# Kernel optimization log

Hardware: AMD Instinct MI355X
Metric: run time of the kernel (lower is better)

## Reference

```python
import jax, jax.numpy as jnp
import numpy as np

NUM_CLASSES = 3
POS_T, NEG_T = 0.5, 0.3
RATIO = 3
W_OBJ, W_CLS, W_LOC = 1.0, 1.0, 2.0


def _pairwise_iou(a, b):
    # a: [N,4] anchors, b: [G,4] gt boxes, xyxy
    ix1 = jnp.maximum(a[:, None, 0], b[None, :, 0])
    iy1 = jnp.maximum(a[:, None, 1], b[None, :, 1])
    ix2 = jnp.minimum(a[:, None, 2], b[None, :, 2])
    iy2 = jnp.minimum(a[:, None, 3], b[None, :, 3])
    inter = jnp.clip(ix2 - ix1, 0) * jnp.clip(iy2 - iy1, 0)
    area_a = (a[:, 2] - a[:, 0]) * (a[:, 3] - a[:, 1])
    area_b = (b[:, 2] - b[:, 0]) * (b[:, 3] - b[:, 1])
    union = area_a[:, None] + area_b[None, :] - inter
    return inter / jnp.maximum(union, 1e-9)


def _masked_mean(x, m):
    c = m.sum()
    return jnp.where(c > 0, (x * m).sum() / jnp.maximum(c, 1.0), 0.0)


def _per_image(pred, anc, ax, ay, aw, ah, boxes_gt, labels_gt):
    # pred: [N, 5+nc]; anc: [N,4]; boxes_gt: [G,4]; labels_gt: [G] in 1..nc
    iou = _pairwise_iou(anc, boxes_gt)              # [N, G]
    best = jnp.argmax(iou, axis=1)
    best_iou = jnp.max(iou, axis=1)
    pos = best_iou >= POS_T
    neg = best_iou < NEG_T
    mb = boxes_gt[best]                             # matched boxes [N,4]
    ml = labels_gt[best]                            # matched labels [N]
    obj_logit = pred[:, 4]
    cls_logit = pred[:, 5:]
    obj_t = pos.astype(pred.dtype)
    # BCEWithLogits (numerically stable)
    obj_loss = jnp.maximum(obj_logit, 0) - obj_logit * obj_t + jnp.log1p(jnp.exp(-jnp.abs(obj_logit)))
    # hard negative mining: top-(3*num_pos) detached obj losses among negatives
    num_pos = pos.sum()
    k = jnp.minimum(RATIO * num_pos, neg.sum())
    cand = jnp.where(neg, jax.lax.stop_gradient(obj_loss), -1.0)
    order = jnp.argsort(-cand)
    ranks = jnp.zeros_like(order).at[order].set(jnp.arange(order.shape[0], dtype=order.dtype))
    sel_neg = neg & (ranks < k)
    loss_obj = _masked_mean(obj_loss, (pos | sel_neg).astype(pred.dtype))
    # classification over positives, labels shifted to 0-based
    logp = jax.nn.log_softmax(cls_logit, axis=-1)
    tgt = jnp.clip(ml - 1, 0)
    ce = -jnp.take_along_axis(logp, tgt[:, None], axis=1)[:, 0]
    loss_cls = _masked_mean(ce, pos.astype(pred.dtype))
    # localization over positives: SmoothL1 on encoded offsets
    gx = (mb[:, 0] + mb[:, 2]) * 0.5
    gy = (mb[:, 1] + mb[:, 3]) * 0.5
    gw = jnp.maximum(mb[:, 2] - mb[:, 0], 1e-6)
    gh = jnp.maximum(mb[:, 3] - mb[:, 1], 1e-6)
    loc_tgt = jnp.stack([(gx - ax) / aw, (gy - ay) / ah,
                         jnp.log(gw / aw), jnp.log(gh / ah)], axis=1)
    d = pred[:, :4] - loc_tgt
    ad = jnp.abs(d)
    sl1 = jnp.where(ad < 1.0, 0.5 * d * d, ad - 0.5)  # [N,4]
    pm = pos.astype(pred.dtype)
    cnt = 4.0 * pm.sum()
    loss_loc = jnp.where(cnt > 0, (sl1 * pm[:, None]).sum() / jnp.maximum(cnt, 1.0), 0.0)
    return loss_obj, loss_cls, loss_loc


def _detection_loss(preds, ancs, gt_boxes, gt_labels):
    B = preds[0].shape[0]
    obj_s = 0.0
    cls_s = 0.0
    loc_s = 0.0
    for pred, anc in zip(preds, ancs):
        Bp, C, H, W = pred.shape
        p = jnp.transpose(pred, (0, 2, 3, 1)).reshape(Bp, -1, 5 + NUM_CLASSES)
        ax = (anc[:, 0] + anc[:, 2]) * 0.5
        ay = (anc[:, 1] + anc[:, 3]) * 0.5
        aw = jnp.maximum(anc[:, 2] - anc[:, 0], 1e-6)
        ah = jnp.maximum(anc[:, 3] - anc[:, 1], 1e-6)
        lo, lc, ll = jax.vmap(
            lambda pb, bb, lb: _per_image(pb, anc, ax, ay, aw, ah, bb, lb)
        )(p, gt_boxes, gt_labels)
        obj_s = obj_s + lo.sum()
        cls_s = cls_s + lc.sum()
        loc_s = loc_s + ll.sum()
    obj_m = obj_s / B
    cls_m = cls_s / B
    loc_m = loc_s / B
    total = W_OBJ * obj_m + W_CLS * cls_m + W_LOC * loc_m
    return total, obj_m, cls_m, loc_m


def setup_inputs() -> dict:
    key = jax.random.key(0)
    k = jax.random.split(key, 8)
    B, G, A = 32, 50, 3
    img = 512.0
    scales = [(128, 128), (64, 64), (32, 32)]
    C = A * (5 + NUM_CLASSES)  # 24

    def make_anchors(H, W):
        stride = img / H
        ys, xs = np.meshgrid(np.arange(H), np.arange(W), indexing="ij")
        cx = (xs + 0.5) * stride
        cy = (ys + 0.5) * stride
        per = []
        for s in (1.0, 1.5, 2.0):
            half = s * stride
            per.append(np.stack([cx - half, cy - half, cx + half, cy + half], axis=-1).reshape(-1, 4))
        b = np.stack(per, axis=1).reshape(-1, 4)  # [H*W*A, 4], A innermost
        return jnp.asarray(b, dtype=jnp.float32)

    preds = [jax.random.normal(k[i], (B, C, H, W), dtype=jnp.float32) for i, (H, W) in enumerate(scales)]
    ancs = [make_anchors(H, W) for (H, W) in scales]
    cx = jax.random.uniform(k[3], (B, G)) * 384.0 + 64.0
    cy = jax.random.uniform(k[4], (B, G)) * 384.0 + 64.0
    w = jax.random.uniform(k[5], (B, G)) * 112.0 + 16.0
    h = jax.random.uniform(k[6], (B, G)) * 112.0 + 16.0
    gt_boxes = jnp.stack([cx - w / 2, cy - h / 2, cx + w / 2, cy + h / 2], axis=-1).astype(jnp.float32)
    gt_labels = jax.random.randint(k[7], (B, G), 1, NUM_CLASSES + 1)
    return {"p0": preds[0], "p1": preds[1], "p2": preds[2],
            "a0": ancs[0], "a1": ancs[1], "a2": ancs[2],
            "gt_boxes": gt_boxes, "gt_labels": gt_labels}


def reference(p0, p1, p2, a0, a1, a2, gt_boxes, gt_labels):
    return _detection_loss([p0, p1, p2], [a0, a1, a2], gt_boxes, gt_labels)
```

## Files before the change

### kernel.cpp

```cpp
#include <hip/hip_runtime.h>

#define WS_ACC_POS   0
#define WS_ACC_NEG   96
#define WS_ACC_OBJ   192
#define WS_ACC_CLS   288
#define WS_ACC_LOC   384
#define WS_SENT      480
#define WS_H1        512
#define WS_TOTAL_U32 (512 + 96*192*2)

#define NBINS        192
#define BIN_OFF      872
#define SUM_SCALE    33554432.0f
#define INV_SUM_SCALE (1.0f/33554432.0f)

__device__ __forceinline__ float sl1f(float d){
  float ad = fabsf(d); return ad < 1.f ? 0.5f*d*d : ad - 0.5f;
}
__device__ __forceinline__ unsigned int rec_cnt(unsigned int v){
  return (v >= 0xA0000000u) ? (v - 0xAAAAAAAAu) : v;
}

__global__ __launch_bounds__(256) void k_main(
    const float* __restrict__ p0, const float* __restrict__ p1, const float* __restrict__ p2,
    const float* __restrict__ gtb, const int* __restrict__ gtl,
    unsigned int* __restrict__ ws)
{
  const int id = blockIdx.x;
  int s, bIm, chunk, H, lw; const float* p;
  if (id < 2048){ s=0; H=128; lw=7; chunk=id>>5;            bIm=id&31;          p=p0; }
  else if (id < 2560){ s=1; H=64; lw=6; chunk=(id-2048)>>5; bIm=(id-2048)&31;   p=p1; }
  else {              s=2; H=32; lw=5; chunk=(id-2560)>>5;  bIm=(id-2560)&31;   p=p2; }
  const int W = H, HW = H*W;
  const float stride = 512.0f/(float)H;
  const int g = s*32 + bIm;
  const int tid = threadIdx.x;

  __shared__ float4 sBox[52];
  __shared__ float  sArea[52], sGx[52], sGy[52], sGw[52], sGh[52];
  __shared__ int    sLbl[52];
  __shared__ int    sNk;
  __shared__ unsigned long long sH[NBINS];
  __shared__ float  sRF[3][4];
  __shared__ unsigned int sRU[2][4];

  if (tid < 64){
    const int ymin = (chunk*256)>>lw;
    const int rowc = 256>>lw;
    const float by1 = ((float)ymin+0.5f)*stride - 2.0f*stride;
    const float by2 = ((float)(ymin+rowc-1)+0.5f)*stride + 2.0f*stride;
    bool keep=false; float4 gb=make_float4(0,0,0,0); int lbl=0;
    if (tid < 50){
      gb  = *(const float4*)(gtb + ((size_t)bIm*50 + tid)*4);
      lbl = gtl[bIm*50 + tid];
      keep = (fminf(by2, gb.w) - fmaxf(by1, gb.y)) > 0.f;
    }
    unsigned long long m = __ballot(keep);
    if (keep){
      int idx = __popcll(m & ((1ull<<tid)-1ull));
      sBox[idx]=gb;
      sArea[idx]=(gb.z-gb.x)*(gb.w-gb.y);
      sGx[idx]=(gb.x+gb.z)*0.5f;  sGy[idx]=(gb.y+gb.w)*0.5f;
      sGw[idx]=fmaxf(gb.z-gb.x,1e-6f); sGh[idx]=fmaxf(gb.w-gb.y,1e-6f);
      sLbl[idx]=lbl;
    }
    if (tid==0) sNk = __popcll(m);
  }
  if (tid < NBINS) sH[tid]=0ull;
  __syncthreads();

  const int nk = sNk;
  const int hw  = chunk*256 + tid;
  const int hwW = chunk*256 + (tid & ~63);
  const int y = hw>>lw, x = hw&(W-1);
  const float cx = ((float)x+0.5f)*stride, cy = ((float)y+0.5f)*stride;

  const float* pb = p + (size_t)bIm*24*HW + hw;
  float xo[3];
  #pragma unroll
  for (int a=0;a<3;a++) xo[a] = pb[(size_t)(a*8+4)*HW];

  const int wxlo = (W >= 64) ? (hwW & (W-1)) : 0;
  const int wxhi = (W >= 64) ? (wxlo + 63)   : (W-1);
  const int wylo = hwW>>lw, wyhi = (hwW+63)>>lw;
  const float m2 = 2.0f*stride;
  const float wx1 = ((float)wxlo+0.5f)*stride - m2;
  const float wx2 = ((float)wxhi+0.5f)*stride + m2;
  const float wy1 = ((float)wylo+0.5f)*stride - m2;
  const float wy2 = ((float)wyhi+0.5f)*stride + m2;

  float half[3]; half[0]=stride; half[1]=1.5f*stride; half[2]=2.0f*stride;
  float areaA[3], bi[3], bu[3]; int bj[3];
  #pragma unroll
  for (int a=0;a<3;a++){
    const float aw = 2.0f*half[a];
    areaA[a]=aw*aw; bi[a]=0.f; bu[a]=1e-9f; bj[a]=0;
  }
  for (int j=0;j<nk;j++){
    const float4 gb = sBox[j];
    if (gb.x >= wx2 || gb.z <= wx1 || gb.y >= wy2 || gb.w <= wy1) continue;
    const float ar = sArea[j];
    #pragma unroll
    for (int a=0;a<3;a++){
      const float iy1 = fmaxf(cy-half[a], gb.y), iy2 = fminf(cy+half[a], gb.w);
      const float ih  = fmaxf(iy2-iy1, 0.f);
      const float ix1 = fmaxf(cx-half[a], gb.x), ix2 = fminf(cx+half[a], gb.z);
      const float iw  = fmaxf(ix2-ix1, 0.f);
      const float inter = iw*ih;
      const float un = areaA[a] + ar - inter;
      if (inter*bu[a] > bi[a]*un){ bi[a]=inter; bu[a]=un; bj[a]=j; }
    }
  }

  int accPos=0, accNeg=0;
  float accObj=0.f, accCls=0.f, accLoc=0.f;
  #pragma unroll
  for (int a=0;a<3;a++){
    const float bestIou = bi[a]/bu[a];
    const bool pos = bestIou >= 0.5f;
    const bool neg = bestIou < 0.3f;
    if (pos || neg){
      float objl = fmaxf(xo[a],0.f) - (pos ? xo[a] : 0.f)
                 + __logf(1.f + __expf(-fabsf(xo[a])));
      objl = fmaxf(objl, 0.f);
      if (neg){
        accNeg++;
        const int bin = min(max((int)(__float_as_uint(objl)>>20) - BIN_OFF, 0), NBINS-1);
        const unsigned long long pack =
            (1ull<<48) | (unsigned long long)__float2uint_rn(objl * SUM_SCALE);
        atomicAdd(&sH[bin], pack);
      } else {
        accPos++; accObj += objl;
        const int jb = bj[a];
        const float aw = 2.0f*half[a];
        const float c0=pb[(size_t)(a*8+5)*HW], c1=pb[(size_t)(a*8+6)*HW], c2=pb[(size_t)(a*8+7)*HW];
        const float mm = fmaxf(fmaxf(c0,c1),c2);
        const float lse = mm + __logf(__expf(c0-mm)+__expf(c1-mm)+__expf(c2-mm));
        const int t = max(sLbl[jb]-1, 0);
        const float ct = (t==0)?c0 : (t==1)?c1 : c2;
        accCls += lse - ct;
        const float tx = (sGx[jb]-cx)/aw;
        const float ty = (sGy[jb]-cy)/aw;
        const float tw = __logf(sGw[jb]/aw);
        const float th = __logf(sGh[jb]/aw);
        accLoc += sl1f(pb[(size_t)(a*8+0)*HW]-tx) + sl1f(pb[(size_t)(a*8+1)*HW]-ty)
                + sl1f(pb[(size_t)(a*8+2)*HW]-tw) + sl1f(pb[(size_t)(a*8+3)*HW]-th);
      }
    }
  }

  #pragma unroll
  for (int o=32;o;o>>=1){
    accPos += __shfl_down(accPos,o,64);
    accNeg += __shfl_down(accNeg,o,64);
    accObj += __shfl_down(accObj,o,64);
    accCls += __shfl_down(accCls,o,64);
    accLoc += __shfl_down(accLoc,o,64);
  }
  if ((tid & 63)==0){
    const int w = tid>>6;
    sRU[0][w]=(unsigned)accPos; sRU[1][w]=(unsigned)accNeg;
    sRF[0][w]=accObj; sRF[1][w]=accCls; sRF[2][w]=accLoc;
  }
  __syncthreads();
  if (tid==0){
    float* wf = (float*)ws;
    unsigned pc=0, nc=0; float ob=0,cl=0,lc=0;
    #pragma unroll
    for (int w=0;w<4;w++){ pc+=sRU[0][w]; nc+=sRU[1][w]; ob+=sRF[0][w]; cl+=sRF[1][w]; lc+=sRF[2][w]; }
    if (pc) atomicAdd(&ws[WS_ACC_POS+g], pc);
    if (nc) atomicAdd(&ws[WS_ACC_NEG+g], nc);
    if (ob!=0.f) atomicAdd(&wf[WS_ACC_OBJ+g], ob);
    if (cl!=0.f) atomicAdd(&wf[WS_ACC_CLS+g], cl);
    if (lc!=0.f) atomicAdd(&wf[WS_ACC_LOC+g], lc);
  }
  if (tid < NBINS){
    const unsigned long long v = sH[tid];
    if (v){
      unsigned long long* gH = (unsigned long long*)(ws + WS_H1) + (size_t)g*NBINS;
      atomicAdd(&gH[tid], v);
    }
  }
}

__global__ __launch_bounds__(64) void k_select(unsigned int* __restrict__ ws,
                                               float* __restrict__ out){
  const int g = blockIdx.x, lane = threadIdx.x;
  float* wf = (float*)ws;
  __shared__ int   sTie, sR;
  __shared__ float sTieAvg;

  const int pos  = (int)rec_cnt(ws[WS_ACC_POS+g]);
  const int negc = (int)rec_cnt(ws[WS_ACC_NEG+g]);
  const int k = min(3*pos, negc);
  float selSum = 0.f;

  if (k > 0){
    const unsigned long long base =
        (ws[WS_SENT]==0xAAAAAAAAu) ? 0xAAAAAAAAAAAAAAAAull : 0ull;
    const unsigned long long* gH =
        (const unsigned long long*)(ws + WS_H1) + (size_t)g*NBINS;
    unsigned int c[3]; float sm[3];
    #pragma unroll
    for (int j=0;j<3;j++){
      const unsigned long long d = gH[lane*3+j] - base;
      c[j]  = (unsigned int)(d>>48);
      sm[j] = (float)(d & 0xFFFFFFFFFFFFull) * INV_SUM_SCALE;
    }
    const unsigned int c3 = c[0]+c[1]+c[2];
    unsigned int incl = c3;
    #pragma unroll
    for (int off=1; off<64; off<<=1){
      unsigned int yv = __shfl_down(incl, off, 64);
      if (lane+off < 64) incl += yv;
    }
    const unsigned int excl = incl - c3;
    if (lane==0){ sTie = -1; sR = 0; sTieAvg = 0.f; }
    if (excl < (unsigned)k && incl >= (unsigned)k){
      unsigned int cum = excl;
      #pragma unroll
      for (int j=2;j>=0;j--){
        const unsigned int cc = c[j];
        if (cum + cc >= (unsigned)k){
          sTie = lane*3+j; sR = (int)((unsigned)k - cum);
          sTieAvg = sm[j]/(float)cc;
          break;
        }
        cum += cc;
      }
    }
    __syncthreads();
    const int tie = sTie;
    float above = 0.f;
    #pragma unroll
    for (int j=0;j<3;j++) if (lane*3+j > tie) above += sm[j];
    #pragma unroll
    for (int o=32;o;o>>=1) above += __shfl_down(above,o,64);
    selSum = above + (float)sR * sTieAvg;
  }
  if (lane==0){
    const int cObj = pos + k;
    const float lo = (cObj>0) ? (wf[WS_ACC_OBJ+g]+selSum)/(float)cObj : 0.f;
    const float lc = (pos>0)  ? wf[WS_ACC_CLS+g]/(float)pos           : 0.f;
    const float ll = (pos>0)  ? wf[WS_ACC_LOC+g]/(float)(4*pos)       : 0.f;
    const float invB = 1.f/32.f;
    atomicAdd(out+0, (lo + lc + 2.f*ll)*invB);
    atomicAdd(out+1, lo*invB);
    atomicAdd(out+2, lc*invB);
    atomicAdd(out+3, ll*invB);
  }
}

extern "C" void kernel_launch(void* const* d_in, const int* in_sizes, int n_in,
                              void* d_out, int out_size, void* d_ws, size_t ws_size,
                              hipStream_t stream){
  if (ws_size < (size_t)WS_TOTAL_U32*4) return;
  const float* p0  = (const float*)d_in[0];
  const float* p1  = (const float*)d_in[1];
  const float* p2  = (const float*)d_in[2];
  const float* gtb = (const float*)d_in[6];
  const int*   gtl = (const int*)d_in[7];
  unsigned int* ws = (unsigned int*)d_ws;
  float* out = (float*)d_out;

  hipLaunchKernelGGL(k_main,   dim3(2688), dim3(256), 0, stream, p0,p1,p2,gtb,gtl,ws);
  hipLaunchKernelGGL(k_select, dim3(96),   dim3(64),  0, stream, ws, out);
}
```

Measured before the change: 122.6 us.

## Process two horizontal pixels per thread with float2 loads, halving grid size

Each thread now handles two adjacent x positions, loading the objectness logits as float2 and reusing the per-gt-box y-overlap and box fetch across both pixels. The grid is halved to match, and each block now covers twice as many rows. The wave-level gt culling drops its x-range test and keeps only the y-range test, so more boxes may go through the IoU loop. The change aims to cut shared-memory box loads, per-block setup and block count, at the cost of more registers per thread and less parallelism.

```diff
diff --git a/kernel.cpp b/kernel.cpp
--- a/kernel.cpp
+++ b/kernel.cpp
@@ -28,10 +28,11 @@
 {
   const int id = blockIdx.x;
   int s, bIm, chunk, H, lw; const float* p;
-  if (id < 2048){ s=0; H=128; lw=7; chunk=id>>5;            bIm=id&31;          p=p0; }
-  else if (id < 2560){ s=1; H=64; lw=6; chunk=(id-2048)>>5; bIm=(id-2048)&31;   p=p1; }
-  else {              s=2; H=32; lw=5; chunk=(id-2560)>>5;  bIm=(id-2560)&31;   p=p2; }
+  if (id < 1024){ s=0; H=128; lw=7; chunk=id>>5;            bIm=id&31;          p=p0; }
+  else if (id < 1280){ s=1; H=64; lw=6; chunk=(id-1024)>>5; bIm=(id-1024)&31;   p=p1; }
+  else {              s=2; H=32; lw=5; chunk=(id-1280)>>5;  bIm=(id-1280)&31;   p=p2; }
   const int W = H, HW = H*W;
+  const int lwp = lw-1, halfW = W>>1;
   const float stride = 512.0f/(float)H;
   const int g = s*32 + bIm;
   const int tid = threadIdx.x;
@@ -45,10 +46,10 @@
   __shared__ unsigned int sRU[2][4];
 
   if (tid < 64){
-    const int ymin = (chunk*256)>>lw;
-    const int rowc = 256>>lw;
+    const int R = 512>>lw;
+    const int ymin = chunk*R;
     const float by1 = ((float)ymin+0.5f)*stride - 2.0f*stride;
-    const float by2 = ((float)(ymin+rowc-1)+0.5f)*stride + 2.0f*stride;
+    const float by2 = ((float)(ymin+R-1)+0.5f)*stride + 2.0f*stride;
     bool keep=false; float4 gb=make_float4(0,0,0,0); int lbl=0;
     if (tid < 50){
       gb  = *(const float4*)(gtb + ((size_t)bIm*50 + tid)*4);
@@ -70,81 +71,92 @@
   __syncthreads();
 
   const int nk = sNk;
-  const int hw  = chunk*256 + tid;
-  const int hwW = chunk*256 + (tid & ~63);
-  const int y = hw>>lw, x = hw&(W-1);
-  const float cx = ((float)x+0.5f)*stride, cy = ((float)y+0.5f)*stride;
-
-  const float* pb = p + (size_t)bIm*24*HW + hw;
-  float xo[3];
-  #pragma unroll
-  for (int a=0;a<3;a++) xo[a] = pb[(size_t)(a*8+4)*HW];
-
-  const int wxlo = (W >= 64) ? (hwW & (W-1)) : 0;
-  const int wxhi = (W >= 64) ? (wxlo + 63)   : (W-1);
-  const int wylo = hwW>>lw, wyhi = (hwW+63)>>lw;
+  const int pairIdx = chunk*256 + tid;
+  const int y  = pairIdx>>lwp;
+  const int x0 = (pairIdx & (halfW-1))<<1;
+  const int hw0 = y*W + x0;
+  const float cx0 = ((float)x0+0.5f)*stride, cy = ((float)y+0.5f)*stride;
+
+  const float* pb = p + (size_t)bIm*24*HW + hw0;
+  float2 xo2[3];
+  #pragma unroll
+  for (int a=0;a<3;a++) xo2[a] = *(const float2*)(pb + (size_t)(a*8+4)*HW);
+
+  const int wbase = chunk*256 + (tid & ~63);
+  const int ylo = wbase>>lwp, yhi = (wbase+63)>>lwp;
   const float m2 = 2.0f*stride;
-  const float wx1 = ((float)wxlo+0.5f)*stride - m2;
-  const float wx2 = ((float)wxhi+0.5f)*stride + m2;
-  const float wy1 = ((float)wylo+0.5f)*stride - m2;
-  const float wy2 = ((float)wyhi+0.5f)*stride + m2;
+  const float wy1 = ((float)ylo+0.5f)*stride - m2;
+  const float wy2 = ((float)yhi+0.5f)*stride + m2;
 
   float half[3]; half[0]=stride; half[1]=1.5f*stride; half[2]=2.0f*stride;
-  float areaA[3], bi[3], bu[3]; int bj[3];
+  float areaA[3], bi[2][3], bu[2][3]; int bj[2][3];
   #pragma unroll
   for (int a=0;a<3;a++){
     const float aw = 2.0f*half[a];
-    areaA[a]=aw*aw; bi[a]=0.f; bu[a]=1e-9f; bj[a]=0;
+    areaA[a]=aw*aw;
+    #pragma unroll
+    for (int i=0;i<2;i++){ bi[i][a]=0.f; bu[i][a]=1e-9f; bj[i][a]=0; }
   }
   for (int j=0;j<nk;j++){
     const float4 gb = sBox[j];
-    if (gb.x >= wx2 || gb.z <= wx1 || gb.y >= wy2 || gb.w <= wy1) continue;
+    if (gb.y >= wy2 || gb.w <= wy1) continue;
     const float ar = sArea[j];
     #pragma unroll
     for (int a=0;a<3;a++){
       const float iy1 = fmaxf(cy-half[a], gb.y), iy2 = fminf(cy+half[a], gb.w);
       const float ih  = fmaxf(iy2-iy1, 0.f);
-      const float ix1 = fmaxf(cx-half[a], gb.x), ix2 = fminf(cx+half[a], gb.z);
-      const float iw  = fmaxf(ix2-ix1, 0.f);
-      const float inter = iw*ih;
-      const float un = areaA[a] + ar - inter;
-      if (inter*bu[a] > bi[a]*un){ bi[a]=inter; bu[a]=un; bj[a]=j; }
+      #pragma unroll
+      for (int i=0;i<2;i++){
+        const float cxi = cx0 + (float)i*stride;
+        const float ix1 = fmaxf(cxi-half[a], gb.x), ix2 = fminf(cxi+half[a], gb.z);
+        const float iw  = fmaxf(ix2-ix1, 0.f);
+        const float inter = iw*ih;
+        const float un = areaA[a] + ar - inter;
+        if (inter*bu[i][a] > bi[i][a]*un){ bi[i][a]=inter; bu[i][a]=un; bj[i][a]=j; }
+      }
     }
   }
 
   int accPos=0, accNeg=0;
   float accObj=0.f, accCls=0.f, accLoc=0.f;
   #pragma unroll
-  for (int a=0;a<3;a++){
-    const float bestIou = bi[a]/bu[a];
-    const bool pos = bestIou >= 0.5f;
-    const bool neg = bestIou < 0.3f;
-    if (pos || neg){
-      float objl = fmaxf(xo[a],0.f) - (pos ? xo[a] : 0.f)
-                 + __logf(1.f + __expf(-fabsf(xo[a])));
-      objl = fmaxf(objl, 0.f);
-      if (neg){
-        accNeg++;
-        const int bin = min(max((int)(__float_as_uint(objl)>>20) - BIN_OFF, 0), NBINS-1);
-        const unsigned long long pack =
-            (1ull<<48) | (unsigned long long)__float2uint_rn(objl * SUM_SCALE);
-        atomicAdd(&sH[bin], pack);
-      } else {
-        accPos++; accObj += objl;
-        const int jb = bj[a];
-        const float aw = 2.0f*half[a];
-        const float c0=pb[(size_t)(a*8+5)*HW], c1=pb[(size_t)(a*8+6)*HW], c2=pb[(size_t)(a*8+7)*HW];
-        const float mm = fmaxf(fmaxf(c0,c1),c2);
-        const float lse = mm + __logf(__expf(c0-mm)+__expf(c1-mm)+__expf(c2-mm));
-        const int t = max(sLbl[jb]-1, 0);
-        const float ct = (t==0)?c0 : (t==1)?c1 : c2;
-        accCls += lse - ct;
-        const float tx = (sGx[jb]-cx)/aw;
-        const float ty = (sGy[jb]-cy)/aw;
-        const float tw = __logf(sGw[jb]/aw);
-        const float th = __logf(sGh[jb]/aw);
-        accLoc += sl1f(pb[(size_t)(a*8+0)*HW]-tx) + sl1f(pb[(size_t)(a*8+1)*HW]-ty)
-                + sl1f(pb[(size_t)(a*8+2)*HW]-tw) + sl1f(pb[(size_t)(a*8+3)*HW]-th);
+  for (int i=0;i<2;i++){
+    const int hw = hw0 + i;
+    const float cxi = cx0 + (float)i*stride;
+    const float* pbi = pb + i;
+    #pragma unroll
+    for (int a=0;a<3;a++){
+      const float bestIou = bi[i][a]/bu[i][a];
+      const bool pos = bestIou >= 0.5f;
+      const bool neg = bestIou < 0.3f;
+      if (pos || neg){
+        const float xo = (i==0) ? xo2[a].x : xo2[a].y;
+        float objl = fmaxf(xo,0.f) - (pos ? xo : 0.f)
+                   + __logf(1.f + __expf(-fabsf(xo)));
+        objl = fmaxf(objl, 0.f);
+        if (neg){
+          accNeg++;
+          const int bin = min(max((int)(__float_as_uint(objl)>>20) - BIN_OFF, 0), NBINS-1);
+          const unsigned long long pack =
+              (1ull<<48) | (unsigned long long)__float2uint_rn(objl * SUM_SCALE);
+          atomicAdd(&sH[bin], pack);
+        } else {
+          accPos++; accObj += objl;
+          const int jb = bj[i][a];
+          const float aw = 2.0f*half[a];
+          const float c0=pbi[(size_t)(a*8+5)*HW], c1=pbi[(size_t)(a*8+6)*HW], c2=pbi[(size_t)(a*8+7)*HW];
+          const float mm = fmaxf(fmaxf(c0,c1),c2);
+          const float lse = mm + __logf(__expf(c0-mm)+__expf(c1-mm)+__expf(c2-mm));
+          const int t = max(sLbl[jb]-1, 0);
+          const float ct = (t==0)?c0 : (t==1)?c1 : c2;
+          accCls += lse - ct;
+          const float tx = (sGx[jb]-cxi)/aw;
+          const float ty = (sGy[jb]-cy )/aw;
+          const float tw = __logf(sGw[jb]/aw);
+          const float th = __logf(sGh[jb]/aw);
+          accLoc += sl1f(pbi[(size_t)(a*8+0)*HW]-tx) + sl1f(pbi[(size_t)(a*8+1)*HW]-ty)
+                  + sl1f(pbi[(size_t)(a*8+2)*HW]-tw) + sl1f(pbi[(size_t)(a*8+3)*HW]-th);
+        }
       }
     }
   }
@@ -263,6 +275,6 @@
   unsigned int* ws = (unsigned int*)d_ws;
   float* out = (float*)d_out;
 
-  hipLaunchKernelGGL(k_main,   dim3(2688), dim3(256), 0, stream, p0,p1,p2,gtb,gtl,ws);
+  hipLaunchKernelGGL(k_main,   dim3(1344), dim3(256), 0, stream, p0,p1,p2,gtb,gtl,ws);
   hipLaunchKernelGGL(k_select, dim3(96),   dim3(64),  0, stream, ws, out);
 }
```

Result: slower. 126.5 us (+3.2%).

## Replace global histogram atomics with per-block histogram slots reduced in select kernel

Applied to the files above, without the earlier changes.

Each main-kernel block now writes its 192-bin histogram to its own workspace slot with plain stores instead of 64-bit atomics into a shared per-group histogram. The select kernel, widened to 256 threads, sums the relevant slots per bin before the prefix scan. This removes atomic contention and the sentinel/base-offset trick. In exchange the workspace grows much larger, and the second kernel does more reads, up to 64 chunks per bin for the first scale.

```diff
diff --git a/kernel.cpp b/kernel.cpp
--- a/kernel.cpp
+++ b/kernel.cpp
@@ -5,9 +5,8 @@
 #define WS_ACC_OBJ   192
 #define WS_ACC_CLS   288
 #define WS_ACC_LOC   384
-#define WS_SENT      480
-#define WS_H1        512
-#define WS_TOTAL_U32 (512 + 96*192*2)
+#define WS_HB        512
+#define WS_TOTAL_U32 (512 + 2688*192*2)
 
 #define NBINS        192
 #define BIN_OFF      872
@@ -175,18 +174,20 @@
     if (lc!=0.f) atomicAdd(&wf[WS_ACC_LOC+g], lc);
   }
   if (tid < NBINS){
-    const unsigned long long v = sH[tid];
-    if (v){
-      unsigned long long* gH = (unsigned long long*)(ws + WS_H1) + (size_t)g*NBINS;
-      atomicAdd(&gH[tid], v);
-    }
-  }
-}
-
-__global__ __launch_bounds__(64) void k_select(unsigned int* __restrict__ ws,
-                                               float* __restrict__ out){
-  const int g = blockIdx.x, lane = threadIdx.x;
+    unsigned long long* hb = (unsigned long long*)(ws + WS_HB) + (size_t)id*NBINS;
+    hb[tid] = sH[tid];
+  }
+}
+
+__global__ __launch_bounds__(256) void k_select(unsigned int* __restrict__ ws,
+                                                float* __restrict__ out){
+  const int g = blockIdx.x, tid = threadIdx.x;
+  const int s = g>>5, bIm = g&31;
+  const int nchunks = (s==0)?64 : (s==1)?16 : 4;
+  const int slot0   = ((s==0)?0 : (s==1)?2048 : 2560) + bIm;
   float* wf = (float*)ws;
+  __shared__ unsigned int hc[NBINS];
+  __shared__ float        hs[NBINS];
   __shared__ int   sTie, sR;
   __shared__ float sTieAvg;
 
@@ -196,49 +197,57 @@
   float selSum = 0.f;
 
   if (k > 0){
-    const unsigned long long base =
-        (ws[WS_SENT]==0xAAAAAAAAu) ? 0xAAAAAAAAAAAAAAAAull : 0ull;
-    const unsigned long long* gH =
-        (const unsigned long long*)(ws + WS_H1) + (size_t)g*NBINS;
-    unsigned int c[3]; float sm[3];
-    #pragma unroll
-    for (int j=0;j<3;j++){
-      const unsigned long long d = gH[lane*3+j] - base;
-      c[j]  = (unsigned int)(d>>48);
-      sm[j] = (float)(d & 0xFFFFFFFFFFFFull) * INV_SUM_SCALE;
-    }
-    const unsigned int c3 = c[0]+c[1]+c[2];
-    unsigned int incl = c3;
-    #pragma unroll
-    for (int off=1; off<64; off<<=1){
-      unsigned int yv = __shfl_down(incl, off, 64);
-      if (lane+off < 64) incl += yv;
-    }
-    const unsigned int excl = incl - c3;
-    if (lane==0){ sTie = -1; sR = 0; sTieAvg = 0.f; }
-    if (excl < (unsigned)k && incl >= (unsigned)k){
-      unsigned int cum = excl;
-      #pragma unroll
-      for (int j=2;j>=0;j--){
-        const unsigned int cc = c[j];
-        if (cum + cc >= (unsigned)k){
-          sTie = lane*3+j; sR = (int)((unsigned)k - cum);
-          sTieAvg = sm[j]/(float)cc;
-          break;
+    if (tid < NBINS){
+      const unsigned long long* hb = (const unsigned long long*)(ws + WS_HB);
+      unsigned int c = 0; float sm = 0.f;
+      for (int cch=0; cch<nchunks; cch++){
+        const unsigned long long v = hb[(size_t)(slot0 + 32*cch)*NBINS + tid];
+        c  += (unsigned int)(v>>48);
+        sm += (float)(v & 0xFFFFFFFFFFFFull) * INV_SUM_SCALE;
+      }
+      hc[tid]=c; hs[tid]=sm;
+    }
+    __syncthreads();
+    if (tid < 64){
+      const int lane = tid;
+      unsigned int c[3]; float sm[3];
+      #pragma unroll
+      for (int j=0;j<3;j++){ c[j]=hc[lane*3+j]; sm[j]=hs[lane*3+j]; }
+      const unsigned int c3 = c[0]+c[1]+c[2];
+      unsigned int incl = c3;
+      #pragma unroll
+      for (int off=1; off<64; off<<=1){
+        unsigned int yv = __shfl_down(incl, off, 64);
+        if (lane+off < 64) incl += yv;
+      }
+      const unsigned int excl = incl - c3;
+      if (lane==0){ sTie = -1; sR = 0; sTieAvg = 0.f; }
+      if (excl < (unsigned)k && incl >= (unsigned)k){
+        unsigned int cum = excl;
+        #pragma unroll
+        for (int j=2;j>=0;j--){
+          const unsigned int cc = c[j];
+          if (cum + cc >= (unsigned)k){
+            sTie = lane*3+j; sR = (int)((unsigned)k - cum);
+            sTieAvg = sm[j]/(float)cc;
+            break;
+          }
+          cum += cc;
         }
-        cum += cc;
       }
     }
     __syncthreads();
-    const int tie = sTie;
-    float above = 0.f;
-    #pragma unroll
-    for (int j=0;j<3;j++) if (lane*3+j > tie) above += sm[j];
-    #pragma unroll
-    for (int o=32;o;o>>=1) above += __shfl_down(above,o,64);
-    selSum = above + (float)sR * sTieAvg;
-  }
-  if (lane==0){
+    if (tid < 64){
+      const int tie = sTie;
+      float above = 0.f;
+      #pragma unroll
+      for (int j=0;j<3;j++) if (tid*3+j > tie) above += hs[tid*3+j];
+      #pragma unroll
+      for (int o=32;o;o>>=1) above += __shfl_down(above,o,64);
+      selSum = above + (float)sR * sTieAvg;
+    }
+  }
+  if (tid==0){
     const int cObj = pos + k;
     const float lo = (cObj>0) ? (wf[WS_ACC_OBJ+g]+selSum)/(float)cObj : 0.f;
     const float lc = (pos>0)  ? wf[WS_ACC_CLS+g]/(float)pos           : 0.f;
@@ -264,5 +273,5 @@
   float* out = (float*)d_out;
 
   hipLaunchKernelGGL(k_main,   dim3(2688), dim3(256), 0, stream, p0,p1,p2,gtb,gtl,ws);
-  hipLaunchKernelGGL(k_select, dim3(96),   dim3(64),  0, stream, ws, out);
-}
+  hipLaunchKernelGGL(k_select, dim3(96),   dim3(256), 0, stream, ws, out);
+}
```

After: 138.1 us. 1.13x slower.
